# Kernel optimization log

Hardware: AMD Instinct MI355X
Metric: run time of the kernel (lower is better)

## Reference

```python
import jax, jax.numpy as jnp
import numpy as np

T = 2048
HID = 2048
H = 16
NOPE = 128
ROPE = 64
QKD = NOPE + ROPE  # 192
VD = 128
QLR = 1536
KVLR = 512
IDX_H = 32
IDX_D = 128
TOPK = 512
EPS = 1e-6
SCALING = QKD ** -0.5


def rms_norm(x, w):
    return x * jax.lax.rsqrt(jnp.mean(x * x, axis=-1, keepdims=True) + EPS) * w


def layer_norm(x, g, b):
    mu = jnp.mean(x, axis=-1, keepdims=True)
    var = jnp.mean((x - mu) ** 2, axis=-1, keepdims=True)
    return (x - mu) * jax.lax.rsqrt(var + EPS) * g + b


def apply_rope(x, positions, base=10000.0):
    # non-neox (interleaved) rotary; x: [..., d] with leading token axis
    d = x.shape[-1]
    inv = 1.0 / (base ** (jnp.arange(0, d, 2, dtype=jnp.float32) / d))
    f = positions.astype(jnp.float32)[:, None] * inv  # [T, d/2]
    shp = (x.shape[0],) + (1,) * (x.ndim - 2) + (d // 2,)
    cos, sin = jnp.cos(f).reshape(shp), jnp.sin(f).reshape(shp)
    x1, x2 = x[..., ::2], x[..., 1::2]
    return jnp.stack([x1 * cos - x2 * sin, x1 * sin + x2 * cos], axis=-1).reshape(x.shape)


def setup_inputs() -> dict:
    key = jax.random.key(0)
    ks = jax.random.split(key, 10)
    s = 0.02
    return {
        "positions": jnp.arange(T, dtype=jnp.int64) if jax.config.jax_enable_x64 else jnp.arange(T, dtype=jnp.int32),
        "hidden_states": jax.random.normal(ks[0], (T, HID), jnp.float32),
        "w_qkv_a": jax.random.normal(ks[1], (HID, QLR + KVLR + ROPE), jnp.float32) * s,
        "q_a_ln_w": jnp.ones((QLR,), jnp.float32),
        "w_qb": jax.random.normal(ks[2], (QLR, H * QKD), jnp.float32) * s,
        "kv_a_ln_w": jnp.ones((KVLR,), jnp.float32),
        "w_kvb": jax.random.normal(ks[3], (KVLR, H * (NOPE + VD)), jnp.float32) * s,
        "w_o": jax.random.normal(ks[4], (H * VD, HID), jnp.float32) * s,
        "w_idx_qb": jax.random.normal(ks[5], (QLR, IDX_H * IDX_D), jnp.float32) * s,
        "w_idx_k": jax.random.normal(ks[6], (HID, IDX_D), jnp.float32) * s,
        "idx_k_gamma": jnp.ones((IDX_D,), jnp.float32),
        "idx_k_beta": jnp.zeros((IDX_D,), jnp.float32),
        "w_wproj": jax.random.normal(ks[7], (HID, IDX_H), jnp.float32) * s,
        "b_wproj": jnp.zeros((IDX_H,), jnp.float32),
    }


def _forward(positions, hidden_states, w_qkv_a, q_a_ln_w, w_qb, kv_a_ln_w, w_kvb,
             w_o, w_idx_qb, w_idx_k, idx_k_gamma, idx_k_beta, w_wproj, b_wproj):
    t = hidden_states.shape[0]
    # fused low-rank projections
    qkv = hidden_states @ w_qkv_a
    q_c, kv_c, k_pe = jnp.split(qkv, [QLR, QLR + KVLR], axis=-1)
    q_c = rms_norm(q_c, q_a_ln_w)           # hidden_states_or_q_c
    kv_cn = rms_norm(kv_c, kv_a_ln_w)

    # ---- Indexer (lightning top-k token selection) ----
    qi = (q_c @ w_idx_qb).reshape(t, IDX_H, IDX_D)
    qi_pe, qi_nope = qi[..., :ROPE], qi[..., ROPE:]
    ki = layer_norm(hidden_states @ w_idx_k, idx_k_gamma, idx_k_beta)  # [T, IDX_D]
    ki_pe, ki_nope = ki[..., :ROPE], ki[..., ROPE:]
    qi = jnp.concatenate([apply_rope(qi_pe, positions), qi_nope], axis=-1)
    ki = jnp.concatenate([apply_rope(ki_pe, positions), ki_nope], axis=-1)
    w = (hidden_states @ w_wproj + b_wproj) * (IDX_D ** -0.5) * (IDX_H ** -0.5)  # [T, IDX_H]
    logits = jax.nn.relu(jnp.einsum('thd,sd->ths', qi, ki))   # [T, IDX_H, T]
    score = jnp.einsum('th,ths->ts', w, logits)               # [T, T]
    causal = jnp.tril(jnp.ones((t, t), bool))
    neg = jnp.finfo(score.dtype).min
    score = jnp.where(causal, score, neg)
    _, topk_idx = jax.lax.top_k(score, TOPK)                  # [T, TOPK]
    sel = jnp.zeros((t, t), bool).at[jnp.arange(t)[:, None], topk_idx].set(True)
    mask = causal & sel

    # ---- MLA attention ----
    q = (q_c @ w_qb).reshape(t, H, QKD)
    q_nope, q_pe = q[..., :NOPE], q[..., NOPE:]
    q_pe = apply_rope(q_pe, positions)
    k_pe_r = apply_rope(k_pe, positions)                      # [T, ROPE], shared across heads
    kv = (kv_cn @ w_kvb).reshape(t, H, NOPE + VD)
    k_nope, v = kv[..., :NOPE], kv[..., NOPE:]
    q_full = jnp.concatenate([q_nope, q_pe], axis=-1)         # [T, H, QKD]
    k_full = jnp.concatenate([k_nope, jnp.broadcast_to(k_pe_r[:, None, :], (t, H, ROPE))], axis=-1)
    attn = jnp.einsum('thd,shd->hts', q_full, k_full) * SCALING
    attn = jnp.where(mask[None], attn, neg)
    p = jax.nn.softmax(attn, axis=-1)
    out = jnp.einsum('hts,shv->thv', p, v).reshape(t, H * VD)
    return out @ w_o


def reference(positions, hidden_states, w_qkv_a, q_a_ln_w, w_qb, kv_a_ln_w, w_kvb,
              w_o, w_idx_qb, w_idx_k, idx_k_gamma, idx_k_beta, w_wproj, b_wproj):
    return _forward(positions, hidden_states, w_qkv_a, q_a_ln_w, w_qb, kv_a_ln_w,
                    w_kvb, w_o, w_idx_qb, w_idx_k, idx_k_gamma, idx_k_beta,
                    w_wproj, b_wproj)
```

## Files before the change

### kernel.cpp

```cpp
#include <hip/hip_runtime.h>
#include <cfloat>
#include <cmath>

#define T_    2048
#define HID_  2048
#define QKVN_ 2112
#define QKVX_ 2272
#define QLR_  1536
#define KVLR_ 512
#define ROPE_ 64
#define NOPE_ 128
#define QKD_  192
#define VD_   128
#define H_    16
#define IDXH_ 32
#define IDXD_ 128
#define TOPK_ 512
#define EPS_  1e-6f
#define SCALING_ 0.07216878364870323f

typedef unsigned int u32;
typedef unsigned short u16;
typedef __bf16 bf16x8 __attribute__((ext_vector_type(8)));
typedef _Float16 f16;
typedef f16 f16x8 __attribute__((ext_vector_type(8)));
typedef float f32x4 __attribute__((ext_vector_type(4)));

__device__ __forceinline__ u16 f2bf(float x) {
  u32 u = __float_as_uint(x);
  u32 r = (u + 0x7fffu + ((u >> 16) & 1u)) >> 16;
  return (u16)r;
}
__device__ __forceinline__ float bf2f(u16 h) { return __uint_as_float(((u32)h) << 16); }
__device__ __forceinline__ u32 pack2(float a, float b) { return (u32)f2bf(a) | ((u32)f2bf(b) << 16); }
__device__ __forceinline__ bf16x8 ld8(const void* p) { return *(const bf16x8*)p; }
__device__ __forceinline__ f32x4 mfma16(bf16x8 a, bf16x8 b, f32x4 c) {
  return __builtin_amdgcn_mfma_f32_16x16x32_bf16(a, b, c, 0, 0, 0);
}
__device__ __forceinline__ u16 hbits(f16 h) { union { f16 h; u16 u; } c; c.h = h; return c.u; }
__device__ __forceinline__ u32 hpack(f16 a, f16 b) { return (u32)hbits(a) | ((u32)hbits(b) << 16); }
__device__ __forceinline__ f16x8 ldh8(const void* p) { return *(const f16x8*)p; }
__device__ __forceinline__ f32x4 mfmah(f16x8 a, f16x8 b, f32x4 c) {
  return __builtin_amdgcn_mfma_f32_16x16x32_f16(a, b, c, 0, 0, 0);
}
__device__ __forceinline__ void gload16(const u16* g, u16* l) {
  __builtin_amdgcn_global_load_lds(
      (__attribute__((address_space(1))) void*)(g),
      (__attribute__((address_space(3))) void*)(l), 16, 0, 0);
}

struct TSJob { const float* src; u16* oh; u16* ol; int K; int N; };
__global__ __launch_bounds__(256) void transpose_split_multi(
    TSJob j0, TSJob j1, TSJob j2, TSJob j3) {
  TSJob jb = (blockIdx.z == 0) ? j0 : (blockIdx.z == 1) ? j1 : (blockIdx.z == 2) ? j2 : j3;
  int k0 = blockIdx.y * 64, n0 = blockIdx.x * 64;
  if (k0 >= jb.K || n0 >= jb.N) return;
  __shared__ float t[64][65];
  for (int j = 0; j < 16; ++j) {
    int u = threadIdx.x + 256 * j; int r = u >> 6, c = u & 63;
    t[r][c] = (k0 + r < jb.K && n0 + c < jb.N) ? jb.src[(size_t)(k0 + r) * jb.N + n0 + c] : 0.f;
  }
  __syncthreads();
  for (int j = 0; j < 16; ++j) {
    int u = threadIdx.x + 256 * j; int r = u >> 6, c = u & 63;
    if (n0 + r < jb.N && k0 + c < jb.K) {
      float v = t[c][r];
      f16 h = (f16)v;
      jb.oh[(size_t)(n0 + r) * jb.K + k0 + c] = hbits(h);
      jb.ol[(size_t)(n0 + r) * jb.K + k0 + c] = hbits((f16)(v - (float)h));
    }
  }
}

struct TBJob { const float* src; u16* out; int K; int N; };
__global__ __launch_bounds__(256) void transpose_bf16_multi(TBJob j0, TBJob j1, TBJob j2) {
  TBJob jb = (blockIdx.z == 0) ? j0 : (blockIdx.z == 1) ? j1 : j2;
  int k0 = blockIdx.y * 64, n0 = blockIdx.x * 64;
  if (k0 >= jb.K || n0 >= jb.N) return;
  __shared__ float t[64][65];
  for (int j = 0; j < 16; ++j) {
    int u = threadIdx.x + 256 * j; int r = u >> 6, c = u & 63;
    t[r][c] = (k0 + r < jb.K && n0 + c < jb.N) ? jb.src[(size_t)(k0 + r) * jb.N + n0 + c] : 0.f;
  }
  __syncthreads();
  for (int j = 0; j < 16; ++j) {
    int u = threadIdx.x + 256 * j; int r = u >> 6, c = u & 63;
    if (n0 + r < jb.N && k0 + c < jb.K) jb.out[(size_t)(n0 + r) * jb.K + k0 + c] = f2bf(t[c][r]);
  }
}

__global__ __launch_bounds__(256) void split_f16_k(
    const float* __restrict__ in, u16* __restrict__ hi, u16* __restrict__ lo, long n) {
  for (long i = ((long)blockIdx.x * 256 + threadIdx.x) * 4; i < n; i += (long)gridDim.x * 1024) {
    float4 v = *(const float4*)(in + i);
    f16 a = (f16)v.x, b = (f16)v.y, c = (f16)v.z, d = (f16)v.w;
    *(u32*)(hi + i) = hpack(a, b);
    *(u32*)(hi + i + 2) = hpack(c, d);
    *(u32*)(lo + i) = hpack((f16)(v.x - (float)a), (f16)(v.y - (float)b));
    *(u32*)(lo + i + 2) = hpack((f16)(v.z - (float)c), (f16)(v.w - (float)d));
  }
}

__global__ __launch_bounds__(256) void conv_bf16_k(
    const float* __restrict__ in, u16* __restrict__ out, long n) {
  for (long i = ((long)blockIdx.x * 256 + threadIdx.x) * 4; i < n; i += (long)gridDim.x * 1024) {
    float4 v = *(const float4*)(in + i);
    *(u32*)(out + i) = pack2(v.x, v.y);
    *(u32*)(out + i + 2) = pack2(v.z, v.w);
  }
}

__global__ __launch_bounds__(256) void gemm_hl(
    const u16* __restrict__ Ah_, const u16* __restrict__ Al_, int lda,
    const u16* __restrict__ Bh_, const u16* __restrict__ Bl_, int ldb,
    float* __restrict__ C, int ldc, const float* __restrict__ bias, int bcol0,
    float bscale, int N, int K) {
  __shared__ u32 Ah[128][16], Al[128][16], Bh[128][16], Bl[128][16];
  const int tid = threadIdx.x;
  const int bm = blockIdx.y * 128, bn = blockIdx.x * 128;
  const int wid = tid >> 6, lane = tid & 63, wr = wid >> 1, wc = wid & 1;
  const int lr = lane & 15, lg = lane >> 4;
  const u16* srcb = (wid == 0) ? Ah_ : (wid == 1) ? Al_ : (wid == 2) ? Bh_ : Bl_;
  const int sld = (wid < 2) ? lda : ldb;
  const int rb = (wid < 2) ? bm : bn;
  u16* dst = (u16*)((wid == 0) ? &Ah[0][0] : (wid == 1) ? &Al[0][0]
                                           : (wid == 2) ? &Bh[0][0] : &Bl[0][0]);
  const int rowl = lane >> 2;
  const int offl = (lane & 3) * 8;
  f32x4 acc[4][4] = {};
  for (int k0 = 0; k0 < K; k0 += 32) {
#pragma unroll
    for (int c = 0; c < 8; ++c) {
      int gr = rb + c * 16 + rowl;
      if (wid >= 2) gr = min(gr, N - 1);
      gload16(srcb + (size_t)gr * sld + k0 + offl, dst + c * 512);
    }
    __syncthreads();
    f16x8 ah[4], al[4], bh[4], bl[4];
#pragma unroll
    for (int i = 0; i < 4; ++i) {
      ah[i] = ldh8(&Ah[wr * 64 + i * 16 + lr][lg * 4]);
      al[i] = ldh8(&Al[wr * 64 + i * 16 + lr][lg * 4]);
      bh[i] = ldh8(&Bh[wc * 64 + i * 16 + lr][lg * 4]);
      bl[i] = ldh8(&Bl[wc * 64 + i * 16 + lr][lg * 4]);
    }
#pragma unroll
    for (int i = 0; i < 4; ++i)
#pragma unroll
      for (int jn = 0; jn < 4; ++jn) {
        acc[i][jn] = mfmah(ah[i], bh[jn], acc[i][jn]);
        acc[i][jn] = mfmah(ah[i], bl[jn], acc[i][jn]);
        acc[i][jn] = mfmah(al[i], bh[jn], acc[i][jn]);
      }
    __syncthreads();
  }
#pragma unroll
  for (int i = 0; i < 4; ++i)
#pragma unroll
    for (int jn = 0; jn < 4; ++jn)
#pragma unroll
      for (int j = 0; j < 4; ++j) {
        int row = bm + wr * 64 + i * 16 + lg * 4 + j;
        int col = bn + wc * 64 + jn * 16 + lr;
        if (col < N) {
          float v = acc[i][jn][j];
          if (col >= bcol0) v = (v + bias[col - bcol0]) * bscale;
          C[(size_t)row * ldc + col] = v;
        }
      }
}

template <int CBF16>
__global__ __launch_bounds__(256) void gemm_t(
    const u16* __restrict__ Ab, int lda, long aoz,
    const u16* __restrict__ Bt, int ldb, long boz,
    void* __restrict__ Cp, int ldc, long coz, int N, int K) {
  __shared__ u32 As[128][16], Bs[128][16];
  const int tid = threadIdx.x;
  const int z = blockIdx.z;
  const int bm = blockIdx.y * 128, bn = blockIdx.x * 128;
  const int wid = tid >> 6, lane = tid & 63, wr = wid >> 1, wc = wid & 1;
  const int lr = lane & 15, lg = lane >> 4;
  const u16* A = Ab + aoz * z;
  const u16* B = Bt + boz * z;
  const u16* srcb = (wid < 2) ? A : B;
  const int sld = (wid < 2) ? lda : ldb;
  const int rb = (wid < 2) ? bm : bn;
  u16* dst = (u16*)((wid < 2) ? &As[0][0] : &Bs[0][0]);
  const int ccb = (wid & 1) * 4;
  const int rowl = lane >> 2;
  const int offl = (lane & 3) * 8;
  f32x4 acc[4][4] = {};
  for (int k0 = 0; k0 < K; k0 += 32) {
#pragma unroll
    for (int c = 0; c < 4; ++c) {
      int cc = ccb + c;
      int gr = rb + cc * 16 + rowl;
      if (wid >= 2) gr = min(gr, N - 1);
      gload16(srcb + (size_t)gr * sld + k0 + offl, dst + cc * 512);
    }
    __syncthreads();
    bf16x8 af[4], bf[4];
#pragma unroll
    for (int i = 0; i < 4; ++i) {
      af[i] = ld8(&As[wr * 64 + i * 16 + lr][lg * 4]);
      bf[i] = ld8(&Bs[wc * 64 + i * 16 + lr][lg * 4]);
    }
#pragma unroll
    for (int i = 0; i < 4; ++i)
#pragma unroll
      for (int jn = 0; jn < 4; ++jn)
        acc[i][jn] = mfma16(af[i], bf[jn], acc[i][jn]);
    __syncthreads();
  }
#pragma unroll
  for (int i = 0; i < 4; ++i)
#pragma unroll
    for (int jn = 0; jn < 4; ++jn)
#pragma unroll
      for (int j = 0; j < 4; ++j) {
        int row = bm + wr * 64 + i * 16 + lg * 4 + j;
        int col = bn + wc * 64 + jn * 16 + lr;
        if (col < N) {
          if (CBF16) ((u16*)Cp)[coz * z + (size_t)row * ldc + col] = f2bf(acc[i][jn][j]);
          else ((float*)Cp)[coz * z + (size_t)row * ldc + col] = acc[i][jn][j];
        }
      }
}

__global__ __launch_bounds__(256) void rmsnorm_kernel(
    const float* __restrict__ qkvx, const float* __restrict__ qw,
    const float* __restrict__ kvw, u16* __restrict__ qcb,
    u16* __restrict__ qch, u16* __restrict__ qcl, u16* __restrict__ kv_cn) {
  const int t = blockIdx.x, tid = threadIdx.x;
  const float* row = qkvx + (size_t)t * QKVX_;
  __shared__ float red[256];
  float ss = 0.f;
  for (int i = tid; i < QLR_; i += 256) { float v = row[i]; ss += v * v; }
  red[tid] = ss; __syncthreads();
  for (int s = 128; s; s >>= 1) { if (tid < s) red[tid] += red[tid + s]; __syncthreads(); }
  float scl = 1.0f / sqrtf(red[0] / (float)QLR_ + EPS_);
  for (int i = tid; i < QLR_; i += 256) {
    float val = row[i] * scl * qw[i];
    qcb[(size_t)t * QLR_ + i] = f2bf(val);
    f16 h = (f16)val;
    qch[(size_t)t * QLR_ + i] = hbits(h);
    qcl[(size_t)t * QLR_ + i] = hbits((f16)(val - (float)h));
  }
  __syncthreads();
  ss = 0.f;
  for (int i = tid; i < KVLR_; i += 256) { float v = row[QLR_ + i]; ss += v * v; }
  red[tid] = ss; __syncthreads();
  for (int s = 128; s; s >>= 1) { if (tid < s) red[tid] += red[tid + s]; __syncthreads(); }
  scl = 1.0f / sqrtf(red[0] / (float)KVLR_ + EPS_);
  for (int i = tid; i < KVLR_; i += 256)
    kv_cn[(size_t)t * KVLR_ + i] = f2bf(row[QLR_ + i] * scl * kvw[i]);
}

__device__ __forceinline__ void rope_pair(float pos, int j, float& x0, float& x1) {
  float inv = powf(10000.f, -(float)j * (1.f / 32.f));
  float f = pos * inv;
  float c = cosf(f), s = sinf(f);
  float a = x0, b = x1;
  x0 = a * c - b * s;
  x1 = a * s + b * c;
}

__global__ __launch_bounds__(256) void rope_qi_split_kernel(
    const float* __restrict__ qi, u16* __restrict__ qih, u16* __restrict__ qil) {
  const int t = blockIdx.x, tid = threadIdx.x;
  float pos = (float)t;
  const float* src = qi + (size_t)t * (IDXH_ * IDXD_);
  u16* dh = qih + (size_t)t * (IDXH_ * IDXD_);
  u16* dl = qil + (size_t)t * (IDXH_ * IDXD_);
  for (int p = tid; p < IDXH_ * IDXD_ / 2; p += 256) {
    int d = p & 63;
    float x0 = src[2 * p], x1 = src[2 * p + 1];
    if (d < 32) rope_pair(pos, d, x0, x1);
    f16 h0 = (f16)x0, h1 = (f16)x1;
    *(u32*)(dh + 2 * p) = hpack(h0, h1);
    *(u32*)(dl + 2 * p) = hpack((f16)(x0 - (float)h0), (f16)(x1 - (float)h1));
  }
}

__global__ __launch_bounds__(256) void rope_q_bf_kernel(u16* __restrict__ qfb) {
  const int t = blockIdx.x, tid = threadIdx.x;
  float pos = (float)t;
  for (int idx = tid; idx < H_ * 32; idx += 256) {
    int hh = idx / 32, j = idx % 32;
    u16* p = qfb + (size_t)t * (H_ * QKD_) + hh * QKD_ + NOPE_ + 2 * j;
    float x0 = bf2f(p[0]), x1 = bf2f(p[1]);
    rope_pair(pos, j, x0, x1);
    p[0] = f2bf(x0); p[1] = f2bf(x1);
  }
}

__global__ __launch_bounds__(64) void rope_kpe_kernel(
    const float* __restrict__ qkvx, u16* __restrict__ kper) {
  const int t = blockIdx.x, tid = threadIdx.x;
  if (tid >= 32) return;
  float pos = (float)t;
  const float* p = qkvx + (size_t)t * QKVX_ + (QLR_ + KVLR_);
  float x0 = p[2 * tid], x1 = p[2 * tid + 1];
  rope_pair(pos, tid, x0, x1);
  kper[(size_t)t * ROPE_ + 2 * tid] = f2bf(x0);
  kper[(size_t)t * ROPE_ + 2 * tid + 1] = f2bf(x1);
}

__global__ __launch_bounds__(128) void ki_ln_rope_kernel(
    const float* __restrict__ qkvx, const float* __restrict__ gamma,
    const float* __restrict__ beta, u16* __restrict__ kih, u16* __restrict__ kil) {
  const int t = blockIdx.x, tid = threadIdx.x;
  __shared__ float x[128];
  __shared__ float red[128];
  float v = qkvx[(size_t)t * QKVX_ + QKVN_ + tid];
  red[tid] = v; __syncthreads();
  for (int s = 64; s; s >>= 1) { if (tid < s) red[tid] += red[tid + s]; __syncthreads(); }
  float mu = red[0] / 128.f;
  __syncthreads();
  float d = v - mu;
  red[tid] = d * d; __syncthreads();
  for (int s = 64; s; s >>= 1) { if (tid < s) red[tid] += red[tid + s]; __syncthreads(); }
  float var = red[0] / 128.f;
  float y = d * (1.0f / sqrtf(var + EPS_)) * gamma[tid] + beta[tid];
  x[tid] = y; __syncthreads();
  float pos = (float)t;
  if (tid < 32) {
    float x0 = x[2 * tid], x1 = x[2 * tid + 1];
    rope_pair(pos, tid, x0, x1);
    x[2 * tid] = x0; x[2 * tid + 1] = x1;
  }
  __syncthreads();
  float fv = x[tid];
  f16 h = (f16)fv;
  kih[(size_t)t * IDXD_ + tid] = hbits(h);
  kil[(size_t)t * IDXD_ + tid] = hbits((f16)(fv - (float)h));
}

__global__ __launch_bounds__(256) void score_mfma(
    const u16* __restrict__ qih, const u16* __restrict__ qil,
    const u16* __restrict__ kih, const u16* __restrict__ kil,
    const float* __restrict__ wgt, int ldw, float* __restrict__ score) {
  const int s0 = blockIdx.x * 64, t0 = blockIdx.y * 64;
  if (s0 > t0 + 63) return;
  __shared__ u32 Kh[64][68], Kl[64][68], Qh[64][68], Ql[64][68];
  __shared__ float wts[64][33];
  const int tid = threadIdx.x;
  const int wid = tid >> 6, lane = tid & 63, wr = wid >> 1, wc = wid & 1;
  const int lr = lane & 15, lg = lane >> 4;
#pragma unroll
  for (int j = 0; j < 4; ++j) {
    int u = tid + 256 * j; int row = u >> 4, p = u & 15;
    *(uint4*)&Kh[row][p * 4] = *(const uint4*)(kih + (size_t)(s0 + row) * IDXD_ + p * 8);
    *(uint4*)&Kl[row][p * 4] = *(const uint4*)(kil + (size_t)(s0 + row) * IDXD_ + p * 8);
  }
#pragma unroll
  for (int j = 0; j < 8; ++j) {
    int u = tid + 256 * j; int r = u >> 5, c = u & 31;
    wts[r][c] = wgt[(size_t)(t0 + r) * ldw + c];
  }
  __syncthreads();
  f16x8 bh[2][4], bl[2][4];
#pragma unroll
  for (int ni = 0; ni < 2; ++ni)
#pragma unroll
    for (int kb = 0; kb < 4; ++kb) {
      bh[ni][kb] = ldh8(&Kh[wc * 32 + ni * 16 + lr][kb * 16 + lg * 4]);
      bl[ni][kb] = ldh8(&Kl[wc * 32 + ni * 16 + lr][kb * 16 + lg * 4]);
    }
  f32x4 fin[2][2] = {};
  for (int h = 0; h < IDXH_; ++h) {
#pragma unroll
    for (int j = 0; j < 4; ++j) {
      int u = tid + 256 * j; int row = u >> 4, p = u & 15;
      size_t g = (size_t)(t0 + row) * (IDXH_ * IDXD_) + h * IDXD_ + p * 8;
      *(uint4*)&Qh[row][p * 4] = *(const uint4*)(qih + g);
      *(uint4*)&Ql[row][p * 4] = *(const uint4*)(qil + g);
    }
    __syncthreads();
    f32x4 acch[2][2] = {};
#pragma unroll
    for (int kb = 0; kb < 4; ++kb) {
      f16x8 ah0 = ldh8(&Qh[wr * 32 + lr][kb * 16 + lg * 4]);
      f16x8 ah1 = ldh8(&Qh[wr * 32 + 16 + lr][kb * 16 + lg * 4]);
      f16x8 al0 = ldh8(&Ql[wr * 32 + lr][kb * 16 + lg * 4]);
      f16x8 al1 = ldh8(&Ql[wr * 32 + 16 + lr][kb * 16 + lg * 4]);
#pragma unroll
      for (int ni = 0; ni < 2; ++ni) {
        acch[0][ni] = mfmah(ah0, bh[ni][kb], acch[0][ni]);
        acch[0][ni] = mfmah(ah0, bl[ni][kb], acch[0][ni]);
        acch[0][ni] = mfmah(al0, bh[ni][kb], acch[0][ni]);
        acch[1][ni] = mfmah(ah1, bh[ni][kb], acch[1][ni]);
        acch[1][ni] = mfmah(ah1, bl[ni][kb], acch[1][ni]);
        acch[1][ni] = mfmah(al1, bh[ni][kb], acch[1][ni]);
      }
    }
#pragma unroll
    for (int mi = 0; mi < 2; ++mi)
#pragma unroll
      for (int j = 0; j < 4; ++j) {
        float w = wts[wr * 32 + mi * 16 + lg * 4 + j][h];
        fin[mi][0][j] += w * fmaxf(acch[mi][0][j], 0.f);
        fin[mi][1][j] += w * fmaxf(acch[mi][1][j], 0.f);
      }
    __syncthreads();
  }
#pragma unroll
  for (int mi = 0; mi < 2; ++mi)
#pragma unroll
    for (int ni = 0; ni < 2; ++ni)
#pragma unroll
      for (int j = 0; j < 4; ++j) {
        int row = t0 + wr * 32 + mi * 16 + lg * 4 + j;
        int col = s0 + wc * 32 + ni * 16 + lr;
        score[(size_t)row * T_ + col] = fin[mi][ni][j];
      }
}

__global__ __launch_bounds__(256) void topk_kernel(
    const float* __restrict__ score, int* __restrict__ selidx,
    int* __restrict__ selcnt) {
  const int t = blockIdx.x;
  const int L = t + 1;
  const int tid = threadIdx.x;
  if (L <= TOPK_) {
    for (int j = tid; j < TOPK_; j += 256)
      selidx[(size_t)t * TOPK_ + j] = (j < L) ? j : 0;
    if (tid == 0) selcnt[t] = L;
    return;
  }
  __shared__ unsigned u[T_];
  __shared__ unsigned hist[16];
  __shared__ unsigned sprefix;
  __shared__ int sk;
  __shared__ int part[256];
  for (int i = tid; i < T_; i += 256) {
    float v = (i < L) ? score[(size_t)t * T_ + i] : -FLT_MAX;
    unsigned b = __float_as_uint(v);
    u[i] = (b & 0x80000000u) ? ~b : (b | 0x80000000u);
  }
  if (tid == 0) { sprefix = 0u; sk = TOPK_; }
  __syncthreads();
  for (int pass = 0; pass < 8; ++pass) {
    const int shift = 28 - 4 * pass;
    if (tid < 16) hist[tid] = 0u;
    __syncthreads();
    unsigned pfx = sprefix;
    for (int i = tid; i < L; i += 256) {
      unsigned val = u[i];
      bool match = (pass == 0) || ((val >> (shift + 4)) == pfx);
      if (match) atomicAdd(&hist[(val >> shift) & 15u], 1u);
    }
    __syncthreads();
    if (tid == 0) {
      int k = sk; unsigned cum = 0u; int bsel = 0;
      for (int bb = 15; bb >= 0; --bb) {
        if (cum + hist[bb] >= (unsigned)k) { bsel = bb; sk = k - (int)cum; break; }
        cum += hist[bb];
      }
      sprefix = (sprefix << 4) | (unsigned)bsel;
    }
    __syncthreads();
  }
  const unsigned thr = sprefix;
  const int kEq = sk;
  const int base = tid * 8;
  int eqloc[8]; int esum = 0;
  for (int r = 0; r < 8; ++r) {
    int i = base + r;
    int f = (i < L && u[i] == thr) ? 1 : 0;
    eqloc[r] = esum; esum += f;
  }
  part[tid] = esum; __syncthreads();
  for (int off = 1; off < 256; off <<= 1) {
    int v = (tid >= off) ? part[tid - off] : 0;
    __syncthreads();
    part[tid] += v;
    __syncthreads();
  }
  const int ebase = (tid > 0) ? part[tid - 1] : 0;
  __syncthreads();
  int sloc[8], selflag[8]; int ssum = 0;
  for (int r = 0; r < 8; ++r) {
    int i = base + r;
    int f = 0;
    if (i < L) {
      unsigned ui = u[i];
      if (ui > thr) f = 1;
      else if (ui == thr && (ebase + eqloc[r]) < kEq) f = 1;
    }
    selflag[r] = f; sloc[r] = ssum; ssum += f;
  }
  part[tid] = ssum; __syncthreads();
  for (int off = 1; off < 256; off <<= 1) {
    int v = (tid >= off) ? part[tid - off] : 0;
    __syncthreads();
    part[tid] += v;
    __syncthreads();
  }
  const int sbase = (tid > 0) ? part[tid - 1] : 0;
  for (int r = 0; r < 8; ++r)
    if (selflag[r]) selidx[(size_t)t * TOPK_ + sbase + sloc[r]] = base + r;
  if (tid == 0) selcnt[t] = TOPK_;
}

__global__ __launch_bounds__(256, 3) void attn_mla_kernel(
    const u16* __restrict__ qeff, const u16* __restrict__ qfb,
    const u16* __restrict__ kvcn, const u16* __restrict__ kper,
    const int* __restrict__ selidx, const int* __restrict__ selcnt,
    u16* __restrict__ Olat) {
  const int t = blockIdx.x;
  const int tid = threadIdx.x;
  const int wid = tid >> 6, lane = tid & 63;
  const int lr = lane & 15, lg = lane >> 4;
  __shared__ int sidxs[512];
  __shared__ u16 Pb[16][520];
  __shared__ u16 Vs[32 * 512];
  __shared__ float redm[4][16];
  __shared__ float reds[4][16];
  const int cnt = selcnt[t];
  for (int j = tid; j < 512; j += 256) sidxs[j] = selidx[(size_t)t * TOPK_ + j];
  __syncthreads();

  int srow[8];
  const u16* kb8[8];
  const u16* kp8[8];
#pragma unroll
  for (int m = 0; m < 8; ++m) {
    srow[m] = sidxs[wid * 128 + m * 16 + lr];
    kb8[m] = kvcn + (size_t)srow[m] * 512 + lg * 8;
    kp8[m] = kper + (size_t)srow[m] * 64 + lg * 8;
  }
  const u16* qe = qeff + (size_t)t * (H_ * 512) + lr * 512 + lg * 8;
  const u16* qp = qfb + (size_t)t * (H_ * QKD_) + lr * QKD_ + NOPE_ + lg * 8;
  f32x4 lgv[8] = {};
  bf16x8 kc[8];
#pragma unroll
  for (int m = 0; m < 8; ++m) kc[m] = ld8(kb8[m]);
#pragma unroll
  for (int kb = 0; kb < 16; ++kb) {
    bf16x8 qfk = ld8(qe + kb * 32);
    bf16x8 kn[8];
#pragma unroll
    for (int m = 0; m < 8; ++m)
      kn[m] = (kb < 15) ? ld8(kb8[m] + (kb + 1) * 32) : ld8(kp8[m]);
#pragma unroll
    for (int m = 0; m < 8; ++m) lgv[m] = mfma16(kc[m], qfk, lgv[m]);
#pragma unroll
    for (int m = 0; m < 8; ++m) kc[m] = kn[m];
  }
  {
    bf16x8 qfk = ld8(qp);
    bf16x8 kn[8];
#pragma unroll
    for (int m = 0; m < 8; ++m) kn[m] = ld8(kp8[m] + 32);
#pragma unroll
    for (int m = 0; m < 8; ++m) lgv[m] = mfma16(kc[m], qfk, lgv[m]);
#pragma unroll
    for (int m = 0; m < 8; ++m) kc[m] = kn[m];
  }
  {
    bf16x8 qfk = ld8(qp + 32);
#pragma unroll
    for (int m = 0; m < 8; ++m) lgv[m] = mfma16(kc[m], qfk, lgv[m]);
  }

  float mx = -FLT_MAX;
#pragma unroll
  for (int m = 0; m < 8; ++m)
#pragma unroll
    for (int j = 0; j < 4; ++j) {
      int slot = wid * 128 + m * 16 + lg * 4 + j;
      float v = (slot < cnt) ? lgv[m][j] * SCALING_ : -FLT_MAX;
      lgv[m][j] = v;
      mx = fmaxf(mx, v);
    }
  mx = fmaxf(mx, __shfl_xor(mx, 16));
  mx = fmaxf(mx, __shfl_xor(mx, 32));
  if (lane < 16) redm[wid][lane] = mx;
  __syncthreads();
  float hm = fmaxf(fmaxf(redm[0][lr], redm[1][lr]), fmaxf(redm[2][lr], redm[3][lr]));
  float sm = 0.f;
#pragma unroll
  for (int m = 0; m < 8; ++m)
#pragma unroll
    for (int j = 0; j < 4; ++j) {
      int slot = wid * 128 + m * 16 + lg * 4 + j;
      float e = (slot < cnt) ? expf(lgv[m][j] - hm) : 0.f;
      lgv[m][j] = e; sm += e;
    }
  sm += __shfl_xor(sm, 16);
  sm += __shfl_xor(sm, 32);
  if (lane < 16) reds[wid][lane] = sm;
  __syncthreads();
  float inv = 1.f / (reds[0][lr] + reds[1][lr] + reds[2][lr] + reds[3][lr]);
#pragma unroll
  for (int m = 0; m < 8; ++m) {
    int sl = wid * 128 + m * 16 + lg * 4;
    *(u32*)&Pb[lr][sl] = pack2(lgv[m][0] * inv, lgv[m][1] * inv);
    *(u32*)&Pb[lr][sl + 2] = pack2(lgv[m][2] * inv, lgv[m][3] * inv);
  }

  f32x4 oacc[8] = {};
  const int colb = wid * 128 + lr;
  for (int c = 0; c < 16; ++c) {
#pragma unroll
    for (int i = 0; i < 8; ++i) {
      int row = i * 4 + wid;
      int s = sidxs[c * 32 + row];
      int piece = lane ^ ((((row >> 3) & 3)) << 1);
      gload16(kvcn + (size_t)s * 512 + piece * 8, &Vs[row * 512]);
    }
    __syncthreads();
    bf16x8 pa = ld8(&Pb[lr][c * 32 + lg * 8]);
#pragma unroll
    for (int C = 0; C < 8; ++C) {
      union { u32 u[4]; bf16x8 v; } bb;
#pragma unroll
      for (int e = 0; e < 4; ++e) {
        int r0 = lg * 8 + 2 * e;
        int sw = ((r0 >> 3) & 3) << 4;
        int base = r0 * 512 + colb + C * 16;
        bb.u[e] = (u32)Vs[base ^ sw] | ((u32)Vs[(base + 512) ^ sw] << 16);
      }
      oacc[C] = mfma16(pa, bb.v, oacc[C]);
    }
    __syncthreads();
  }
#pragma unroll
  for (int C = 0; C < 8; ++C)
#pragma unroll
    for (int j = 0; j < 4; ++j) {
      int h = lg * 4 + j;
      Olat[(size_t)t * (H_ * 512) + h * 512 + wid * 128 + C * 16 + lr] = f2bf(oacc[C][j]);
    }
}

extern "C" void kernel_launch(void* const* d_in, const int* in_sizes, int n_in,
                              void* d_out, int out_size, void* d_ws, size_t ws_size,
                              hipStream_t stream) {
  const float* hidden    = (const float*)d_in[1];
  const float* w_qkv_a   = (const float*)d_in[2];
  const float* q_a_ln_w  = (const float*)d_in[3];
  const float* w_qb      = (const float*)d_in[4];
  const float* kv_a_ln_w = (const float*)d_in[5];
  const float* w_kvb     = (const float*)d_in[6];
  const float* w_o       = (const float*)d_in[7];
  const float* w_idx_qb  = (const float*)d_in[8];
  const float* w_idx_k   = (const float*)d_in[9];
  const float* idx_g     = (const float*)d_in[10];
  const float* idx_b     = (const float*)d_in[11];
  const float* w_wproj   = (const float*)d_in[12];
  const float* b_wproj   = (const float*)d_in[13];

  char* W = (char*)d_ws;
  size_t o = 0;
  auto alloc = [&](size_t bytes) { void* p = W + o; o += (bytes + 255) & ~(size_t)255; return p; };
  u16* qcb     = (u16*)alloc((size_t)T_ * QLR_ * 2);
  u16* kv_cn   = (u16*)alloc((size_t)T_ * KVLR_ * 2);
  u16* kper    = (u16*)alloc((size_t)T_ * ROPE_ * 2);
  int* selidx  = (int*)alloc((size_t)T_ * TOPK_ * 4);
  int* selcnt  = (int*)alloc((size_t)T_ * 4);
  u16* kih     = (u16*)alloc((size_t)T_ * IDXD_ * 2);
  u16* kil     = (u16*)alloc((size_t)T_ * IDXD_ * 2);
  u16* hidh    = (u16*)alloc((size_t)T_ * HID_ * 2);
  u16* hidl    = (u16*)alloc((size_t)T_ * HID_ * 2);
  u16* qch     = (u16*)alloc((size_t)T_ * QLR_ * 2);
  u16* qcl     = (u16*)alloc((size_t)T_ * QLR_ * 2);
  u16* wiqh    = (u16*)alloc((size_t)(IDXH_ * IDXD_) * QLR_ * 2);
  u16* wiql    = (u16*)alloc((size_t)(IDXH_ * IDXD_) * QLR_ * 2);
  u16* qih     = qch;
  u16* qil     = qch + (size_t)T_ * IDXH_ * IDXD_;
  float* qi    = (float*)alloc((size_t)T_ * IDXH_ * IDXD_ * 4);
  u16* qeff    = (u16*)qi;
  float* score = (float*)alloc((size_t)T_ * T_ * 4);
  u16* qfb     = (u16*)score;
  u16* attno   = (u16*)score;
  u16* wcath   = (u16*)alloc((size_t)QKVX_ * HID_ * 2);
  u16* wcatl   = (u16*)alloc((size_t)QKVX_ * HID_ * 2);
  float* qkvx  = (float*)alloc((size_t)T_ * QKVX_ * 4);
  u16* Olat    = wcath;
  u16* wqbt    = (u16*)alloc((size_t)(H_ * QKD_) * QLR_ * 2);
  u16* wkvb    = (u16*)alloc((size_t)KVLR_ * (H_ * 256) * 2);
  u16* wkvbt   = (u16*)alloc((size_t)(H_ * 256) * KVLR_ * 2);
  u16* wot     = (u16*)alloc((size_t)(H_ * VD_) * HID_ * 2);

  dim3 blk(256);
  auto g2 = [](int M, int N, int Z) { return dim3((N + 127) / 128, M / 128, Z); };

  {
    TSJob j0{w_qkv_a, wcath, wcatl, HID_, QKVN_};
    TSJob j1{w_idx_qb, wiqh, wiql, QLR_, IDXH_ * IDXD_};
    TSJob j2{w_idx_k, wcath + (size_t)QKVN_ * HID_, wcatl + (size_t)QKVN_ * HID_, HID_, IDXD_};
    TSJob j3{w_wproj, wcath + (size_t)(QKVN_ + IDXD_) * HID_, wcatl + (size_t)(QKVN_ + IDXD_) * HID_, HID_, IDXH_};
    transpose_split_multi<<<dim3(64, 32, 4), blk, 0, stream>>>(j0, j1, j2, j3);
  }
  {
    TBJob j0{w_qb, wqbt, QLR_, H_ * QKD_};
    TBJob j1{w_kvb, wkvbt, KVLR_, H_ * 256};
    TBJob j2{w_o, wot, H_ * VD_, HID_};
    transpose_bf16_multi<<<dim3(64, 32, 3), blk, 0, stream>>>(j0, j1, j2);
  }
  split_f16_k<<<2048, blk, 0, stream>>>(hidden, hidh, hidl, (long)T_ * HID_);
  conv_bf16_k<<<2048, blk, 0, stream>>>(w_kvb, wkvb, (long)KVLR_ * H_ * 256);

  gemm_hl<<<g2(T_, QKVX_, 1), blk, 0, stream>>>(
      hidh, hidl, HID_, wcath, wcatl, HID_, qkvx, QKVX_,
      b_wproj, QKVN_ + IDXD_, 0.015625f, QKVX_, HID_);
  rmsnorm_kernel<<<T_, blk, 0, stream>>>(qkvx, q_a_ln_w, kv_a_ln_w, qcb, qch, qcl, kv_cn);
  rope_kpe_kernel<<<T_, 64, 0, stream>>>(qkvx, kper);
  ki_ln_rope_kernel<<<T_, 128, 0, stream>>>(qkvx, idx_g, idx_b, kih, kil);

  gemm_hl<<<g2(T_, IDXH_ * IDXD_, 1), blk, 0, stream>>>(
      qch, qcl, QLR_, wiqh, wiql, QLR_, qi, IDXH_ * IDXD_,
      nullptr, 1 << 30, 1.f, IDXH_ * IDXD_, QLR_);
  rope_qi_split_kernel<<<T_, blk, 0, stream>>>(qi, qih, qil);

  score_mfma<<<dim3(32, 32), blk, 0, stream>>>(qih, qil, kih, kil,
                                               qkvx + QKVN_ + IDXD_, QKVX_, score);
  topk_kernel<<<T_, blk, 0, stream>>>(score, selidx, selcnt);

  gemm_t<1><<<g2(T_, H_ * QKD_, 1), blk, 0, stream>>>(qcb, QLR_, 0, wqbt, QLR_, 0, qfb, H_ * QKD_, 0, H_ * QKD_, QLR_);
  rope_q_bf_kernel<<<T_, blk, 0, stream>>>(qfb);
  gemm_t<1><<<g2(T_, 512, H_), blk, 0, stream>>>(qfb, H_ * QKD_, QKD_, wkvb, H_ * 256, 256, qeff, H_ * 512, 512, 512, NOPE_);
  attn_mla_kernel<<<T_, blk, 0, stream>>>(qeff, qfb, kv_cn, kper, selidx, selcnt, Olat);
  gemm_t<1><<<g2(T_, VD_, H_), blk, 0, stream>>>(Olat, H_ * 512, 512, wkvbt + 128 * 512, KVLR_, 256 * 512, attno, H_ * VD_, VD_, VD_, 512);
  gemm_t<0><<<g2(T_, HID_, 1), blk, 0, stream>>>(attno, H_ * VD_, 0, wot, H_ * VD_, 0, d_out, HID_, 0, HID_, H_ * VD_);
}
```

Before: 712.0 us.

## Give each wave a private V slice and prefetch the next chunk during MFMA

In the MLA attention P·V loop, the shared 32x512 V tile is replaced by per-wave 32x128 slices, and each wave loads only the latent columns it consumes. This removes the block-wide __syncthreads around every chunk. The next chunk's global-to-LDS loads are issued after the B fragments are read into registers, so they overlap with the MFMAs, which now run at raised priority. The cost is more registers for the eight held B fragments, and correctness now depends on explicit waitcnt ordering instead of barriers.

```diff
diff --git a/kernel.cpp b/kernel.cpp
--- a/kernel.cpp
+++ b/kernel.cpp
@@ -515,7 +515,7 @@
   const int lr = lane & 15, lg = lane >> 4;
   __shared__ int sidxs[512];
   __shared__ u16 Pb[16][520];
-  __shared__ u16 Vs[32 * 512];
+  __shared__ u16 Vw[4][32][128];
   __shared__ float redm[4][16];
   __shared__ float reds[4][16];
   const int cnt = selcnt[t];
@@ -600,32 +600,50 @@
     *(u32*)&Pb[lr][sl] = pack2(lgv[m][0] * inv, lgv[m][1] * inv);
     *(u32*)&Pb[lr][sl + 2] = pack2(lgv[m][2] * inv, lgv[m][3] * inv);
   }
-
+  __syncthreads();
+
+  const int klq = lane >> 4;
+  const int pq = lane & 15;
+  u16* vbase = &Vw[wid][0][0];
   f32x4 oacc[8] = {};
-  const int colb = wid * 128 + lr;
+#pragma unroll
+  for (int j = 0; j < 8; ++j) {
+    int kl = j * 4 + klq;
+    int s = sidxs[kl];
+    int srcp = pq ^ (kl >> 3);
+    gload16(kvcn + (size_t)s * 512 + wid * 128 + srcp * 8, vbase + j * 512);
+  }
   for (int c = 0; c < 16; ++c) {
-#pragma unroll
-    for (int i = 0; i < 8; ++i) {
-      int row = i * 4 + wid;
-      int s = sidxs[c * 32 + row];
-      int piece = lane ^ ((((row >> 3) & 3)) << 1);
-      gload16(kvcn + (size_t)s * 512 + piece * 8, &Vs[row * 512]);
-    }
-    __syncthreads();
+    asm volatile("s_waitcnt vmcnt(0)" ::: "memory");
+    __builtin_amdgcn_sched_barrier(0);
     bf16x8 pa = ld8(&Pb[lr][c * 32 + lg * 8]);
+    union BB { u32 u[4]; bf16x8 v; };
+    BB bb[8];
 #pragma unroll
     for (int C = 0; C < 8; ++C) {
-      union { u32 u[4]; bf16x8 v; } bb;
 #pragma unroll
       for (int e = 0; e < 4; ++e) {
-        int r0 = lg * 8 + 2 * e;
-        int sw = ((r0 >> 3) & 3) << 4;
-        int base = r0 * 512 + colb + C * 16;
-        bb.u[e] = (u32)Vs[base ^ sw] | ((u32)Vs[(base + 512) ^ sw] << 16);
-      }
-      oacc[C] = mfma16(pa, bb.v, oacc[C]);
-    }
-    __syncthreads();
+        int k0 = lg * 8 + 2 * e;
+        int dloc = C * 16 + lr;
+        int sp = (((dloc >> 3) ^ lg) << 3) + (dloc & 7);
+        bb[C].u[e] = (u32)Vw[wid][k0][sp] | ((u32)Vw[wid][k0 + 1][sp] << 16);
+      }
+    }
+    asm volatile("s_waitcnt lgkmcnt(0)" ::: "memory");
+    __builtin_amdgcn_sched_barrier(0);
+    if (c < 15) {
+#pragma unroll
+      for (int j = 0; j < 8; ++j) {
+        int kl = j * 4 + klq;
+        int s = sidxs[(c + 1) * 32 + kl];
+        int srcp = pq ^ (kl >> 3);
+        gload16(kvcn + (size_t)s * 512 + wid * 128 + srcp * 8, vbase + j * 512);
+      }
+    }
+    __builtin_amdgcn_s_setprio(1);
+#pragma unroll
+    for (int C = 0; C < 8; ++C) oacc[C] = mfma16(pa, bb[C].v, oacc[C]);
+    __builtin_amdgcn_s_setprio(0);
   }
 #pragma unroll
   for (int C = 0; C < 8; ++C)
```

After: 714.7 us. Within noise of the previous version (+0.4%).
